# Kernel optimization log

Hardware: AMD Instinct MI355X
Metric: run time of the kernel (lower is better)

Reference implementation:

```python
import jax, jax.numpy as jnp
import numpy as np

SHAPE = (32, 512, 512)  # (D, H, W) dense voxel grid
N_ACTIVE = 150000


def setup_inputs() -> dict:
    key = jax.random.key(0)
    k_f, k_w1, k_w2 = jax.random.split(key, 3)
    D, H, W = SHAPE
    # unique active voxel coordinates (collision-free dense-grid hash)
    rng = np.random.default_rng(0)
    lin = rng.permutation(D * H * W)[:N_ACTIVE]
    z = lin // (H * W)
    y = (lin // W) % H
    x = lin % W
    coors = np.stack([np.zeros(N_ACTIVE, np.int32), z.astype(np.int32),
                      y.astype(np.int32), x.astype(np.int32)], axis=1)
    features = jax.random.normal(k_f, (N_ACTIVE, 3), dtype=jnp.float32)
    # per-offset GEMM weights: [K^3, Cin, Cout]
    w1 = jax.random.normal(k_w1, (27, 3, 128), dtype=jnp.float32) * 0.2
    w2 = jax.random.normal(k_w2, (27, 128, 128), dtype=jnp.float32) * 0.05
    return {"features": features, "coors": jnp.asarray(coors), "w1": w1,
            "w2": w2, "batch_size": 1}


def _build_grid(coors):
    D, H, W = SHAPE
    n = coors.shape[0]
    grid = jnp.full((D, H, W), -1, dtype=jnp.int32)
    return grid.at[coors[:, 1], coors[:, 2], coors[:, 3]].set(
        jnp.arange(n, dtype=jnp.int32))


def _subm_conv3d(feat, coors, grid, w):
    """Submanifold 3x3x3 conv: gather active neighbors per offset, GEMM, accumulate.
    feat: [N, Cin]; w: [27, Cin, Cout]; output defined only on active sites -> [N, Cout]."""
    D, H, W = SHAPE
    n = feat.shape[0]
    out = jnp.zeros((n, w.shape[-1]), dtype=feat.dtype)
    k = 0
    for dz in (-1, 0, 1):
        for dy in (-1, 0, 1):
            for dx in (-1, 0, 1):
                nz = coors[:, 1] + dz
                ny = coors[:, 2] + dy
                nx = coors[:, 3] + dx
                inb = ((nz >= 0) & (nz < D) & (ny >= 0) & (ny < H)
                       & (nx >= 0) & (nx < W))
                nidx = grid[jnp.clip(nz, 0, D - 1), jnp.clip(ny, 0, H - 1),
                            jnp.clip(nx, 0, W - 1)]
                valid = inb & (nidx >= 0)
                g = jnp.where(valid[:, None],
                              feat[jnp.clip(nidx, 0, n - 1)], 0.0)  # [N, Cin]
                out = out + g @ w[k]
                k += 1
    return out


def reference(features, coors, w1, w2, batch_size):
    # SparseConvTensor: features [N,3], coors [N,4] (batch,z,y,x), batch_size=1
    grid = _build_grid(coors)
    h = _subm_conv3d(features, coors, grid, w1)   # SubMConv3d(3, 128, 3)
    out = _subm_conv3d(h, coors, grid, w2)        # SubMConv3d(128, 128, 3), shared indice_key
    return out
```

## Files before the change

### kernel.cpp

```cpp
#include <hip/hip_runtime.h>
#include <stdint.h>

#define GD 32
#define GH 512
#define GW 512
#define GDHW (GD * GH * GW)
#define KOFF 27
#define CAP 4096
#define CNTS 32
#define NW2 (KOFF * 128 * 128)

typedef __attribute__((ext_vector_type(8))) short short8;
typedef __attribute__((ext_vector_type(4))) float f32x4;

__device__ __forceinline__ unsigned short f32_to_bf16(float x) {
    unsigned int u = __float_as_uint(x);
    unsigned int r = (u + 0x7FFFu + ((u >> 16) & 1u)) >> 16;
    return (unsigned short)r;
}

__global__ __launch_bounds__(256) void setup_kernel(
    const int* __restrict__ coors, int* __restrict__ grid,
    unsigned int* __restrict__ bitgrid,
    const float* __restrict__ w2, unsigned short* __restrict__ w2t,
    int n, int nbsc) {
    const int bid = blockIdx.x, t = threadIdx.x;
    if (bid < nbsc) {
        int i = bid * 256 + t;
        if (i < n) {
            int z = coors[i * 4 + 1];
            int y = coors[i * 4 + 2];
            int x = coors[i * 4 + 3];
            int cell = (z * GH + y) * GW + x;
            grid[cell] = i;
            atomicOr(&bitgrid[cell >> 5], 1u << (cell & 31));
        }
    } else {
        int g = (bid - nbsc) * 256 + t;
        if (g < NW2) {
            int k = g >> 14;
            int c = (g >> 7) & 127;
            int q = g & 127;
            w2t[g] = f32_to_bf16(w2[(k * 128 + q) * 128 + c]);
        }
    }
}

__global__ __launch_bounds__(256) void nbr1_kernel(
    const int* __restrict__ coors, const int* __restrict__ grid,
    const unsigned int* __restrict__ bitgrid,
    int* __restrict__ vcnt, int* __restrict__ nbrc,
    unsigned long long* __restrict__ wmask, int* __restrict__ bcnt,
    int n, int nb) {
    __shared__ int wcnt[4][26];

    const int bid = blockIdx.x;
    const int i = bid * 256 + threadIdx.x;
    const int t = threadIdx.x, wave = t >> 6, lane = t & 63;
    const bool live = (i < n);

    int z = 0, y = 0, x = 0;
    if (live) {
        z = coors[i * 4 + 1];
        y = coors[i * 4 + 2];
        x = coors[i * 4 + 3];
    }

    int c0r[9];
    bool rowok[9];
    unsigned int wlo[9], whi[9];
#pragma unroll
    for (int r = 0; r < 9; ++r) {
        int dz = r / 3 - 1, dy = r % 3 - 1;
        int nz = z + dz, ny = y + dy;
        int cz = min(max(nz, 0), GD - 1);
        int cy = min(max(ny, 0), GH - 1);
        int c0 = (cz * GH + cy) * GW + x;
        c0r[r] = c0;
        rowok[r] = live && nz >= 0 && nz < GD && ny >= 0 && ny < GH;
        wlo[r] = bitgrid[(c0 - 1) >> 5];
        whi[r] = bitgrid[(c0 + 1) >> 5];
    }

    unsigned int mask26 = 0;
    int c = 0;
#pragma unroll
    for (int k = 0; k < 27; ++k) {
        if (k == 13) continue;
        int r = k / 3, dx = k % 3 - 1;
        int nx = x + dx;
        int cell = c0r[r] + dx;
        bool ok = rowok[r] && nx >= 0 && nx < GW;
        unsigned int w;
        if (dx < 0) w = wlo[r];
        else if (dx > 0) w = whi[r];
        else w = ((cell & 31) == 0) ? whi[r] : wlo[r];
        bool occ = ok && ((w >> (cell & 31)) & 1u);
        if (occ) {
            int jj = grid[cell];
            nbrc[i * 27 + c] = (k << 20) | jj;
            ++c;
            mask26 |= 1u << (k - (k > 13));
        }
    }
    if (live) vcnt[i] = c;

#pragma unroll
    for (int kk = 0; kk < 26; ++kk) {
        unsigned long long m = __ballot((mask26 >> kk) & 1u);
        if (lane == 0) {
            wmask[((size_t)bid * 4 + wave) * 26 + kk] = m;
            wcnt[wave][kk] = __popcll(m);
        }
    }
    __syncthreads();
    if (t < 26)
        bcnt[t * nb + bid] = wcnt[0][t] + wcnt[1][t] + wcnt[2][t] + wcnt[3][t];
}

__global__ __launch_bounds__(256) void scan_conv1_kernel(
    const int* __restrict__ bcnt, int* __restrict__ bbase,
    int* __restrict__ cnts, int nb,
    const float* __restrict__ feat, const float* __restrict__ w1,
    const int* __restrict__ vcnt, const int* __restrict__ nbrc,
    unsigned short* __restrict__ hout, int n) {
    const int t = threadIdx.x;
    if (blockIdx.x < 26) {
        const int k = blockIdx.x;
        __shared__ int s[256];
        int run = 0;
        for (int base = 0; base < nb; base += 256) {
            int idx = base + t;
            int v = (idx < nb) ? bcnt[k * nb + idx] : 0;
            s[t] = v;
            __syncthreads();
            for (int off = 1; off < 256; off <<= 1) {
                int u = (t >= off) ? s[t - off] : 0;
                __syncthreads();
                s[t] += u;
                __syncthreads();
            }
            int incl = s[t];
            int total = s[255];
            if (idx < nb) bbase[k * nb + idx] = run + incl - v;
            run += total;
            __syncthreads();
        }
        if (t == 0) cnts[k * CNTS] = run;
        return;
    }
    const int wave = t >> 6, lane = t & 63;
    const int i = (blockIdx.x - 26) * 4 + wave;
    if (i >= n) return;
    const int c2 = lane * 2;

    const int cnt = vcnt[i];
    float f0 = feat[i * 3 + 0];
    float f1 = feat[i * 3 + 1];
    float f2 = feat[i * 3 + 2];

    const float* wc = w1 + 13 * 384 + c2;
    float2 w0 = *(const float2*)(wc);
    float2 wv1 = *(const float2*)(wc + 128);
    float2 w2_ = *(const float2*)(wc + 256);
    float a0 = f0 * w0.x + f1 * wv1.x + f2 * w2_.x;
    float a1 = f0 * w0.y + f1 * wv1.y + f2 * w2_.y;

    for (int s = 0; s < cnt; ++s) {
        int e = nbrc[i * 27 + s];
        int k = e >> 20, jj = e & 0xFFFFF;
        float g0 = feat[jj * 3 + 0];
        float g1 = feat[jj * 3 + 1];
        float g2 = feat[jj * 3 + 2];
        const float* wk = w1 + k * 384 + c2;
        float2 u0 = *(const float2*)(wk);
        float2 u1 = *(const float2*)(wk + 128);
        float2 u2 = *(const float2*)(wk + 256);
        a0 += g0 * u0.x + g1 * u1.x + g2 * u2.x;
        a1 += g0 * u0.y + g1 * u1.y + g2 * u2.y;
    }

    unsigned int packed = (unsigned int)f32_to_bf16(a0) |
                          ((unsigned int)f32_to_bf16(a1) << 16);
    *(unsigned int*)(hout + (size_t)i * 128 + c2) = packed;
}

__global__ __launch_bounds__(256) void nbr2_kernel(
    const int* __restrict__ vcnt, const int* __restrict__ nbrc,
    const unsigned long long* __restrict__ wmask,
    const int* __restrict__ bbase,
    int* __restrict__ pairs, int* __restrict__ npos, int n, int nb) {
    __shared__ unsigned long long lmsk[4][26];
    __shared__ int woff[4][26];
    __shared__ int bb[26];

    const int bid = blockIdx.x;
    const int t = threadIdx.x, wave = t >> 6, lane = t & 63;
    if (t < 26) {
        unsigned long long m0 = wmask[((size_t)bid * 4 + 0) * 26 + t];
        unsigned long long m1 = wmask[((size_t)bid * 4 + 1) * 26 + t];
        unsigned long long m2 = wmask[((size_t)bid * 4 + 2) * 26 + t];
        unsigned long long m3 = wmask[((size_t)bid * 4 + 3) * 26 + t];
        lmsk[0][t] = m0; lmsk[1][t] = m1; lmsk[2][t] = m2; lmsk[3][t] = m3;
        int p0 = __popcll(m0), p1 = __popcll(m1), p2 = __popcll(m2);
        woff[0][t] = 0; woff[1][t] = p0; woff[2][t] = p0 + p1;
        woff[3][t] = p0 + p1 + p2;
        bb[t] = bbase[t * nb + bid];
    }
    __syncthreads();

    const int i = bid * 256 + t;
    if (i >= n) return;
    const unsigned long long lmask = (1ull << lane) - 1;
    const int cnt = vcnt[i];
    for (int s = 0; s < cnt; ++s) {
        int e = nbrc[i * 27 + s];
        int k = e >> 20, j = e & 0xFFFFF;
        int kk = k - (k > 13);
        int pos = bb[kk] + woff[wave][kk] + __popcll(lmsk[wave][kk] & lmask);
        if (pos < CAP) {
            pairs[kk * CAP + pos] = j;
            npos[i * 27 + s] = kk * CAP + pos;
        } else {
            npos[i * 27 + s] = -1;
        }
    }
}

__global__ __launch_bounds__(256, 2) void conv2ab_kernel(
    const unsigned short* __restrict__ h,
    const unsigned short* __restrict__ w2t,
    const int* __restrict__ pairs, const int* __restrict__ cnts,
    unsigned short* __restrict__ corr,
    float* __restrict__ out, int n) {
    const int t = threadIdx.x;
    const int wave = t >> 6, lane = t & 63;
    const int lane16 = lane & 15, quad = lane >> 4;
    const int wm = wave >> 1, wn = wave & 1;

    if (blockIdx.x < 26 * 32) {
        const int kb = blockIdx.x >> 5;
        const int tile = blockIdx.x & 31;
        const int cnt = min(cnts[kb * CNTS], CAP);
        const int base = tile * 128;
        if (base >= cnt) return;
        const int m = min(128, cnt - base);
        const int k = kb + (kb >= 13);
        const int* pk = pairs + kb * CAP + base;

        short8 a[4][4];
#pragma unroll
        for (int ms = 0; ms < 4; ++ms) {
            int r = wm * 64 + ms * 16 + lane16;
            bool v = (r < m);
            int j = v ? pk[r] : 0;
            const unsigned short* hp = h + (size_t)j * 128 + quad * 8;
#pragma unroll
            for (int ks = 0; ks < 4; ++ks)
                a[ms][ks] = v ? *(const short8*)(hp + ks * 32)
                              : (short8){0, 0, 0, 0, 0, 0, 0, 0};
        }

        short8 b[4][4];
        const unsigned short* wbase = w2t + (size_t)k * 16384 + quad * 8;
#pragma unroll
        for (int ns = 0; ns < 4; ++ns) {
            int c = wn * 64 + ns * 16 + lane16;
            const unsigned short* wp = wbase + c * 128;
#pragma unroll
            for (int ks = 0; ks < 4; ++ks)
                b[ns][ks] = *(const short8*)(wp + ks * 32);
        }

        f32x4 acc[4][4];
#pragma unroll
        for (int p = 0; p < 4; ++p)
#pragma unroll
            for (int q = 0; q < 4; ++q) acc[p][q] = (f32x4){0.f, 0.f, 0.f, 0.f};

#pragma unroll
        for (int ks = 0; ks < 4; ++ks)
#pragma unroll
            for (int ns = 0; ns < 4; ++ns)
#pragma unroll
                for (int ms = 0; ms < 4; ++ms)
                    acc[ms][ns] = __builtin_amdgcn_mfma_f32_16x16x32_bf16(
                        a[ms][ks], b[ns][ks], acc[ms][ns], 0, 0, 0);

#pragma unroll
        for (int ms = 0; ms < 4; ++ms) {
#pragma unroll
            for (int r = 0; r < 4; ++r) {
                int row = wm * 64 + ms * 16 + quad * 4 + r;
                if (row < m) {
                    unsigned short* cr =
                        corr + (size_t)(kb * CAP + base + row) * 128;
#pragma unroll
                    for (int ns = 0; ns < 4; ++ns) {
                        int col = wn * 64 + ns * 16 + lane16;
                        cr[col] = f32_to_bf16(acc[ms][ns][r]);
                    }
                }
            }
        }
        return;
    }

    const int row0 = (blockIdx.x - 26 * 32) * 128;

    short8 a[4][4];
#pragma unroll
    for (int ms = 0; ms < 4; ++ms) {
        int r = row0 + wm * 64 + ms * 16 + lane16;
        r = min(r, n - 1);
        const unsigned short* hp = h + (size_t)r * 128 + quad * 8;
#pragma unroll
        for (int ks = 0; ks < 4; ++ks)
            a[ms][ks] = *(const short8*)(hp + ks * 32);
    }

    short8 b[4][4];
    const unsigned short* wbase = w2t + 13 * 16384 + quad * 8;
#pragma unroll
    for (int ns = 0; ns < 4; ++ns) {
        int c = wn * 64 + ns * 16 + lane16;
        const unsigned short* wp = wbase + c * 128;
#pragma unroll
        for (int ks = 0; ks < 4; ++ks)
            b[ns][ks] = *(const short8*)(wp + ks * 32);
    }

    f32x4 acc[4][4];
#pragma unroll
    for (int p = 0; p < 4; ++p)
#pragma unroll
        for (int q = 0; q < 4; ++q) acc[p][q] = (f32x4){0.f, 0.f, 0.f, 0.f};

#pragma unroll
    for (int ks = 0; ks < 4; ++ks)
#pragma unroll
        for (int ns = 0; ns < 4; ++ns)
#pragma unroll
            for (int ms = 0; ms < 4; ++ms)
                acc[ms][ns] = __builtin_amdgcn_mfma_f32_16x16x32_bf16(
                    a[ms][ks], b[ns][ks], acc[ms][ns], 0, 0, 0);

#pragma unroll
    for (int ms = 0; ms < 4; ++ms) {
#pragma unroll
        for (int r = 0; r < 4; ++r) {
            int i = row0 + wm * 64 + ms * 16 + quad * 4 + r;
            if (i < n) {
#pragma unroll
                for (int ns = 0; ns < 4; ++ns) {
                    int col = wn * 64 + ns * 16 + lane16;
                    out[(size_t)i * 128 + col] = acc[ms][ns][r];
                }
            }
        }
    }
}

__global__ __launch_bounds__(256) void fixup_kernel(
    const unsigned short* __restrict__ corr, const int* __restrict__ vcnt,
    const int* __restrict__ npos, float* __restrict__ out, int n) {
    const int i = blockIdx.x * 4 + (threadIdx.x >> 6);
    const int lane = threadIdx.x & 63;
    if (i >= n) return;
    const int cnt = vcnt[i];
    if (cnt == 0) return;
    const int* np = npos + i * 27;

    float a0 = 0.f, a1 = 0.f;
    for (int s = 0; s < cnt; ++s) {
        int p = np[s];
        if (p >= 0) {
            unsigned int u =
                *(const unsigned int*)(corr + (size_t)p * 128 + lane * 2);
            a0 += __uint_as_float(u << 16);
            a1 += __uint_as_float(u & 0xFFFF0000u);
        }
    }
    float2* op = (float2*)(out + (size_t)i * 128) + lane;
    float2 cur = *op;
    cur.x += a0;
    cur.y += a1;
    *op = cur;
}

extern "C" void kernel_launch(void* const* d_in, const int* in_sizes, int n_in,
                              void* d_out, int out_size, void* d_ws,
                              size_t ws_size, hipStream_t stream) {
    const float* feat = (const float*)d_in[0];
    const int* coors = (const int*)d_in[1];
    const float* w1 = (const float*)d_in[2];
    const float* w2 = (const float*)d_in[3];
    float* out = (float*)d_out;

    const int n = in_sizes[0] / 3;
    const int nb = (n + 255) / 256;

    uint8_t* ws = (uint8_t*)d_ws;
    size_t off = 0;
    int* grid = (int*)(ws + off); off += (size_t)GDHW * 4;
    unsigned int* bitgrid = (unsigned int*)(ws + off);
    off += (size_t)(GDHW / 8);
    int* vcnt = (int*)(ws + off); off += (size_t)n * 4;
    int* nbrc = (int*)(ws + off); off += (size_t)n * 27 * 4;
    int* npos = (int*)(ws + off); off += (size_t)n * 27 * 4;
    off = (off + 255) & ~(size_t)255;
    unsigned long long* wmask = (unsigned long long*)(ws + off);
    off += (size_t)nb * 4 * 26 * 8;
    int* bcnt = (int*)(ws + off); off += (size_t)26 * nb * 4;
    int* bbase = (int*)(ws + off); off += (size_t)26 * nb * 4;
    off = (off + 255) & ~(size_t)255;
    unsigned short* hbuf = (unsigned short*)(ws + off);
    off += (size_t)n * 128 * 2;
    off = (off + 255) & ~(size_t)255;
    unsigned short* w2t = (unsigned short*)(ws + off);
    off += (size_t)KOFF * 128 * 128 * 2;
    off = (off + 255) & ~(size_t)255;
    int* pairs = (int*)(ws + off);
    off += (size_t)26 * CAP * 4;
    off = (off + 255) & ~(size_t)255;
    int* cnts = (int*)(ws + off); off += 26 * CNTS * 4;
    off = (off + 255) & ~(size_t)255;
    unsigned short* corr = (unsigned short*)(ws + off);
    off += (size_t)26 * CAP * 128 * 2;

    hipMemsetAsync(bitgrid, 0x00, (size_t)(GDHW / 8), stream);

    const int nbw2 = (NW2 + 255) / 256;
    setup_kernel<<<nb + nbw2, 256, 0, stream>>>(coors, grid, bitgrid, w2, w2t,
                                                n, nb);
    nbr1_kernel<<<nb, 256, 0, stream>>>(coors, grid, bitgrid, vcnt, nbrc,
                                        wmask, bcnt, n, nb);
    scan_conv1_kernel<<<26 + (n + 3) / 4, 256, 0, stream>>>(
        bcnt, bbase, cnts, nb, feat, w1, vcnt, nbrc, hbuf, n);
    nbr2_kernel<<<nb, 256, 0, stream>>>(vcnt, nbrc, wmask, bbase, pairs, npos,
                                        n, nb);
    conv2ab_kernel<<<26 * 32 + (n + 127) / 128, 256, 0, stream>>>(
        hbuf, w2t, pairs, cnts, corr, out, n);
    fixup_kernel<<<(n + 3) / 4, 256, 0, stream>>>(corr, vcnt, npos, out, n);
}
```

Baseline: 228.2 us.

## Fuse scan into nbr1 via last-block pattern, merge fixup into conv2a

```diff
diff --git a/kernel.cpp b/kernel.cpp
--- a/kernel.cpp
+++ b/kernel.cpp
@@ -51,8 +51,10 @@
     const unsigned int* __restrict__ bitgrid,
     int* __restrict__ vcnt, int* __restrict__ nbrc,
     unsigned long long* __restrict__ wmask, int* __restrict__ bcnt,
+    int* __restrict__ bbase, int* __restrict__ cnts, int* __restrict__ done,
     int n, int nb) {
     __shared__ int wcnt[4][26];
+    __shared__ int sdone;
 
     const int bid = blockIdx.x;
     const int i = bid * 256 + threadIdx.x;
@@ -116,41 +118,83 @@
     __syncthreads();
     if (t < 26)
         bcnt[t * nb + bid] = wcnt[0][t] + wcnt[1][t] + wcnt[2][t] + wcnt[3][t];
-}
-
-__global__ __launch_bounds__(256) void scan_conv1_kernel(
-    const int* __restrict__ bcnt, int* __restrict__ bbase,
-    int* __restrict__ cnts, int nb,
+
+    __syncthreads();
+    __threadfence();
+    if (t == 0) sdone = atomicAdd(done, 1);
+    __syncthreads();
+    if (sdone != nb - 1) return;
+    __threadfence();
+
+    const int nchunk = (nb + 63) / 64;
+    for (int k = wave; k < 26; k += 4) {
+        int running = 0;
+        for (int ch = 0; ch < nchunk; ++ch) {
+            int idx = ch * 64 + lane;
+            int v = (idx < nb) ? bcnt[k * nb + idx] : 0;
+            int orig = v;
+#pragma unroll
+            for (int off = 1; off < 64; off <<= 1) {
+                int u = __shfl_up(v, off);
+                if (lane >= off) v += u;
+            }
+            if (idx < nb) bbase[k * nb + idx] = running + v - orig;
+            running += __shfl(v, 63);
+        }
+        if (lane == 0) cnts[k * CNTS] = running;
+    }
+}
+
+__global__ __launch_bounds__(256) void nbr2_conv1_kernel(
+    const int* __restrict__ vcnt, const int* __restrict__ nbrc,
+    const unsigned long long* __restrict__ wmask,
+    const int* __restrict__ bbase,
+    int* __restrict__ pairs, int* __restrict__ npos,
     const float* __restrict__ feat, const float* __restrict__ w1,
-    const int* __restrict__ vcnt, const int* __restrict__ nbrc,
-    unsigned short* __restrict__ hout, int n) {
+    unsigned short* __restrict__ hout, int n, int nb) {
     const int t = threadIdx.x;
-    if (blockIdx.x < 26) {
-        const int k = blockIdx.x;
-        __shared__ int s[256];
-        int run = 0;
-        for (int base = 0; base < nb; base += 256) {
-            int idx = base + t;
-            int v = (idx < nb) ? bcnt[k * nb + idx] : 0;
-            s[t] = v;
-            __syncthreads();
-            for (int off = 1; off < 256; off <<= 1) {
-                int u = (t >= off) ? s[t - off] : 0;
-                __syncthreads();
-                s[t] += u;
-                __syncthreads();
+    const int wave = t >> 6, lane = t & 63;
+
+    if (blockIdx.x < (unsigned)nb) {
+        __shared__ unsigned long long lmsk[4][26];
+        __shared__ int woff[4][26];
+        __shared__ int bb[26];
+
+        const int bid = blockIdx.x;
+        if (t < 26) {
+            unsigned long long m0 = wmask[((size_t)bid * 4 + 0) * 26 + t];
+            unsigned long long m1 = wmask[((size_t)bid * 4 + 1) * 26 + t];
+            unsigned long long m2 = wmask[((size_t)bid * 4 + 2) * 26 + t];
+            unsigned long long m3 = wmask[((size_t)bid * 4 + 3) * 26 + t];
+            lmsk[0][t] = m0; lmsk[1][t] = m1; lmsk[2][t] = m2; lmsk[3][t] = m3;
+            int p0 = __popcll(m0), p1 = __popcll(m1), p2 = __popcll(m2);
+            woff[0][t] = 0; woff[1][t] = p0; woff[2][t] = p0 + p1;
+            woff[3][t] = p0 + p1 + p2;
+            bb[t] = bbase[t * nb + bid];
+        }
+        __syncthreads();
+
+        const int i = bid * 256 + t;
+        if (i >= n) return;
+        const unsigned long long lmask = (1ull << lane) - 1;
+        const int cnt = vcnt[i];
+        for (int s = 0; s < cnt; ++s) {
+            int e = nbrc[i * 27 + s];
+            int k = e >> 20, j = e & 0xFFFFF;
+            int kk = k - (k > 13);
+            int pos = bb[kk] + woff[wave][kk] +
+                      __popcll(lmsk[wave][kk] & lmask);
+            if (pos < CAP) {
+                pairs[kk * CAP + pos] = j;
+                npos[i * 27 + s] = kk * CAP + pos;
+            } else {
+                npos[i * 27 + s] = -1;
             }
-            int incl = s[t];
-            int total = s[255];
-            if (idx < nb) bbase[k * nb + idx] = run + incl - v;
-            run += total;
-            __syncthreads();
-        }
-        if (t == 0) cnts[k * CNTS] = run;
+        }
         return;
     }
-    const int wave = t >> 6, lane = t & 63;
-    const int i = (blockIdx.x - 26) * 4 + wave;
+
+    const int i = (blockIdx.x - nb) * 4 + wave;
     if (i >= n) return;
     const int c2 = lane * 2;
 
@@ -185,128 +229,93 @@
     *(unsigned int*)(hout + (size_t)i * 128 + c2) = packed;
 }
 
-__global__ __launch_bounds__(256) void nbr2_kernel(
-    const int* __restrict__ vcnt, const int* __restrict__ nbrc,
-    const unsigned long long* __restrict__ wmask,
-    const int* __restrict__ bbase,
-    int* __restrict__ pairs, int* __restrict__ npos, int n, int nb) {
-    __shared__ unsigned long long lmsk[4][26];
-    __shared__ int woff[4][26];
-    __shared__ int bb[26];
-
-    const int bid = blockIdx.x;
-    const int t = threadIdx.x, wave = t >> 6, lane = t & 63;
-    if (t < 26) {
-        unsigned long long m0 = wmask[((size_t)bid * 4 + 0) * 26 + t];
-        unsigned long long m1 = wmask[((size_t)bid * 4 + 1) * 26 + t];
-        unsigned long long m2 = wmask[((size_t)bid * 4 + 2) * 26 + t];
-        unsigned long long m3 = wmask[((size_t)bid * 4 + 3) * 26 + t];
-        lmsk[0][t] = m0; lmsk[1][t] = m1; lmsk[2][t] = m2; lmsk[3][t] = m3;
-        int p0 = __popcll(m0), p1 = __popcll(m1), p2 = __popcll(m2);
-        woff[0][t] = 0; woff[1][t] = p0; woff[2][t] = p0 + p1;
-        woff[3][t] = p0 + p1 + p2;
-        bb[t] = bbase[t * nb + bid];
-    }
-    __syncthreads();
-
-    const int i = bid * 256 + t;
-    if (i >= n) return;
-    const unsigned long long lmask = (1ull << lane) - 1;
-    const int cnt = vcnt[i];
-    for (int s = 0; s < cnt; ++s) {
-        int e = nbrc[i * 27 + s];
-        int k = e >> 20, j = e & 0xFFFFF;
-        int kk = k - (k > 13);
-        int pos = bb[kk] + woff[wave][kk] + __popcll(lmsk[wave][kk] & lmask);
-        if (pos < CAP) {
-            pairs[kk * CAP + pos] = j;
-            npos[i * 27 + s] = kk * CAP + pos;
-        } else {
-            npos[i * 27 + s] = -1;
-        }
-    }
-}
-
-__global__ __launch_bounds__(256, 2) void conv2ab_kernel(
+__global__ __launch_bounds__(256, 2) void conv2b_kernel(
     const unsigned short* __restrict__ h,
     const unsigned short* __restrict__ w2t,
     const int* __restrict__ pairs, const int* __restrict__ cnts,
-    unsigned short* __restrict__ corr,
+    unsigned short* __restrict__ corr) {
+    const int kb = blockIdx.x >> 5;
+    const int tile = blockIdx.x & 31;
+    const int cnt = min(cnts[kb * CNTS], CAP);
+    const int base = tile * 128;
+    if (base >= cnt) return;
+    const int m = min(128, cnt - base);
+    const int k = kb + (kb >= 13);
+    const int* pk = pairs + kb * CAP + base;
+
+    const int t = threadIdx.x;
+    const int wave = t >> 6, lane = t & 63;
+    const int lane16 = lane & 15, quad = lane >> 4;
+    const int wm = wave >> 1, wn = wave & 1;
+
+    short8 a[4][4];
+#pragma unroll
+    for (int ms = 0; ms < 4; ++ms) {
+        int r = wm * 64 + ms * 16 + lane16;
+        bool v = (r < m);
+        int j = v ? pk[r] : 0;
+        const unsigned short* hp = h + (size_t)j * 128 + quad * 8;
+#pragma unroll
+        for (int ks = 0; ks < 4; ++ks)
+            a[ms][ks] = v ? *(const short8*)(hp + ks * 32)
+                          : (short8){0, 0, 0, 0, 0, 0, 0, 0};
+    }
+
+    short8 b[4][4];
+    const unsigned short* wbase = w2t + (size_t)k * 16384 + quad * 8;
+#pragma unroll
+    for (int ns = 0; ns < 4; ++ns) {
+        int c = wn * 64 + ns * 16 + lane16;
+        const unsigned short* wp = wbase + c * 128;
+#pragma unroll
+        for (int ks = 0; ks < 4; ++ks)
+            b[ns][ks] = *(const short8*)(wp + ks * 32);
+    }
+
+    f32x4 acc[4][4];
+#pragma unroll
+    for (int p = 0; p < 4; ++p)
+#pragma unroll
+        for (int q = 0; q < 4; ++q) acc[p][q] = (f32x4){0.f, 0.f, 0.f, 0.f};
+
+#pragma unroll
+    for (int ks = 0; ks < 4; ++ks)
+#pragma unroll
+        for (int ns = 0; ns < 4; ++ns)
+#pragma unroll
+            for (int ms = 0; ms < 4; ++ms)
+                acc[ms][ns] = __builtin_amdgcn_mfma_f32_16x16x32_bf16(
+                    a[ms][ks], b[ns][ks], acc[ms][ns], 0, 0, 0);
+
+#pragma unroll
+    for (int ms = 0; ms < 4; ++ms) {
+#pragma unroll
+        for (int r = 0; r < 4; ++r) {
+            int row = wm * 64 + ms * 16 + quad * 4 + r;
+            if (row < m) {
+                unsigned short* cr =
+                    corr + (size_t)(kb * CAP + base + row) * 128;
+#pragma unroll
+                for (int ns = 0; ns < 4; ++ns) {
+                    int col = wn * 64 + ns * 16 + lane16;
+                    cr[col] = f32_to_bf16(acc[ms][ns][r]);
+                }
+            }
+        }
+    }
+}
+
+__global__ __launch_bounds__(256, 2) void conv2a_fix_kernel(
+    const unsigned short* __restrict__ h,
+    const unsigned short* __restrict__ w2t,
+    const int* __restrict__ vcnt, const int* __restrict__ npos,
+    const unsigned short* __restrict__ corr,
     float* __restrict__ out, int n) {
     const int t = threadIdx.x;
     const int wave = t >> 6, lane = t & 63;
     const int lane16 = lane & 15, quad = lane >> 4;
     const int wm = wave >> 1, wn = wave & 1;
-
-    if (blockIdx.x < 26 * 32) {
-        const int kb = blockIdx.x >> 5;
-        const int tile = blockIdx.x & 31;
-        const int cnt = min(cnts[kb * CNTS], CAP);
-        const int base = tile * 128;
-        if (base >= cnt) return;
-        const int m = min(128, cnt - base);
-        const int k = kb + (kb >= 13);
-        const int* pk = pairs + kb * CAP + base;
-
-        short8 a[4][4];
-#pragma unroll
-        for (int ms = 0; ms < 4; ++ms) {
-            int r = wm * 64 + ms * 16 + lane16;
-            bool v = (r < m);
-            int j = v ? pk[r] : 0;
-            const unsigned short* hp = h + (size_t)j * 128 + quad * 8;
-#pragma unroll
-            for (int ks = 0; ks < 4; ++ks)
-                a[ms][ks] = v ? *(const short8*)(hp + ks * 32)
-                              : (short8){0, 0, 0, 0, 0, 0, 0, 0};
-        }
-
-        short8 b[4][4];
-        const unsigned short* wbase = w2t + (size_t)k * 16384 + quad * 8;
-#pragma unroll
-        for (int ns = 0; ns < 4; ++ns) {
-            int c = wn * 64 + ns * 16 + lane16;
-            const unsigned short* wp = wbase + c * 128;
-#pragma unroll
-            for (int ks = 0; ks < 4; ++ks)
-                b[ns][ks] = *(const short8*)(wp + ks * 32);
-        }
-
-        f32x4 acc[4][4];
-#pragma unroll
-        for (int p = 0; p < 4; ++p)
-#pragma unroll
-            for (int q = 0; q < 4; ++q) acc[p][q] = (f32x4){0.f, 0.f, 0.f, 0.f};
-
-#pragma unroll
-        for (int ks = 0; ks < 4; ++ks)
-#pragma unroll
-            for (int ns = 0; ns < 4; ++ns)
-#pragma unroll
-                for (int ms = 0; ms < 4; ++ms)
-                    acc[ms][ns] = __builtin_amdgcn_mfma_f32_16x16x32_bf16(
-                        a[ms][ks], b[ns][ks], acc[ms][ns], 0, 0, 0);
-
-#pragma unroll
-        for (int ms = 0; ms < 4; ++ms) {
-#pragma unroll
-            for (int r = 0; r < 4; ++r) {
-                int row = wm * 64 + ms * 16 + quad * 4 + r;
-                if (row < m) {
-                    unsigned short* cr =
-                        corr + (size_t)(kb * CAP + base + row) * 128;
-#pragma unroll
-                    for (int ns = 0; ns < 4; ++ns) {
-                        int col = wn * 64 + ns * 16 + lane16;
-                        cr[col] = f32_to_bf16(acc[ms][ns][r]);
-                    }
-                }
-            }
-        }
-        return;
-    }
-
-    const int row0 = (blockIdx.x - 26 * 32) * 128;
+    const int row0 = blockIdx.x * 128;
 
     short8 a[4][4];
 #pragma unroll
@@ -351,6 +360,20 @@
         for (int r = 0; r < 4; ++r) {
             int i = row0 + wm * 64 + ms * 16 + quad * 4 + r;
             if (i < n) {
+                const int cnt = vcnt[i];
+                const int* np = npos + i * 27;
+                for (int s = 0; s < cnt; ++s) {
+                    int p = np[s];
+                    if (p >= 0) {
+                        const unsigned short* cr =
+                            corr + (size_t)p * 128 + wn * 64 + lane16;
+#pragma unroll
+                        for (int ns = 0; ns < 4; ++ns) {
+                            unsigned int uv = cr[ns * 16];
+                            acc[ms][ns][r] += __uint_as_float(uv << 16);
+                        }
+                    }
+                }
 #pragma unroll
                 for (int ns = 0; ns < 4; ++ns) {
                     int col = wn * 64 + ns * 16 + lane16;
@@ -359,33 +382,6 @@
             }
         }
     }
-}
-
-__global__ __launch_bounds__(256) void fixup_kernel(
-    const unsigned short* __restrict__ corr, const int* __restrict__ vcnt,
-    const int* __restrict__ npos, float* __restrict__ out, int n) {
-    const int i = blockIdx.x * 4 + (threadIdx.x >> 6);
-    const int lane = threadIdx.x & 63;
-    if (i >= n) return;
-    const int cnt = vcnt[i];
-    if (cnt == 0) return;
-    const int* np = npos + i * 27;
-
-    float a0 = 0.f, a1 = 0.f;
-    for (int s = 0; s < cnt; ++s) {
-        int p = np[s];
-        if (p >= 0) {
-            unsigned int u =
-                *(const unsigned int*)(corr + (size_t)p * 128 + lane * 2);
-            a0 += __uint_as_float(u << 16);
-            a1 += __uint_as_float(u & 0xFFFF0000u);
-        }
-    }
-    float2* op = (float2*)(out + (size_t)i * 128) + lane;
-    float2 cur = *op;
-    cur.x += a0;
-    cur.y += a1;
-    *op = cur;
 }
 
 extern "C" void kernel_launch(void* const* d_in, const int* in_sizes, int n_in,
@@ -405,6 +401,7 @@
     int* grid = (int*)(ws + off); off += (size_t)GDHW * 4;
     unsigned int* bitgrid = (unsigned int*)(ws + off);
     off += (size_t)(GDHW / 8);
+    int* done = (int*)(ws + off); off += 256;
     int* vcnt = (int*)(ws + off); off += (size_t)n * 4;
     int* nbrc = (int*)(ws + off); off += (size_t)n * 27 * 4;
     int* npos = (int*)(ws + off); off += (size_t)n * 27 * 4;
@@ -428,18 +425,16 @@
     unsigned short* corr = (unsigned short*)(ws + off);
     off += (size_t)26 * CAP * 128 * 2;
 
-    hipMemsetAsync(bitgrid, 0x00, (size_t)(GDHW / 8), stream);
+    hipMemsetAsync(bitgrid, 0x00, (size_t)(GDHW / 8) + 256, stream);
 
     const int nbw2 = (NW2 + 255) / 256;
     setup_kernel<<<nb + nbw2, 256, 0, stream>>>(coors, grid, bitgrid, w2, w2t,
                                                 n, nb);
     nbr1_kernel<<<nb, 256, 0, stream>>>(coors, grid, bitgrid, vcnt, nbrc,
-                                        wmask, bcnt, n, nb);
-    scan_conv1_kernel<<<26 + (n + 3) / 4, 256, 0, stream>>>(
-        bcnt, bbase, cnts, nb, feat, w1, vcnt, nbrc, hbuf, n);
-    nbr2_kernel<<<nb, 256, 0, stream>>>(vcnt, nbrc, wmask, bbase, pairs, npos,
-                                        n, nb);
-    conv2ab_kernel<<<26 * 32 + (n + 127) / 128, 256, 0, stream>>>(
-        hbuf, w2t, pairs, cnts, corr, out, n);
-    fixup_kernel<<<(n + 3) / 4, 256, 0, stream>>>(corr, vcnt, npos, out, n);
-}
+                                        wmask, bcnt, bbase, cnts, done, n, nb);
+    nbr2_conv1_kernel<<<nb + (n + 3) / 4, 256, 0, stream>>>(
+        vcnt, nbrc, wmask, bbase, pairs, npos, feat, w1, hbuf, n, nb);
+    conv2b_kernel<<<26 * 32, 256, 0, stream>>>(hbuf, w2t, pairs, cnts, corr);
+    conv2a_fix_kernel<<<(n + 127) / 128, 256, 0, stream>>>(
+        hbuf, w2t, vcnt, npos, corr, out, n);
+}
```

New measurement: 331.2 us. 1.45x slower.
